# Performance work log

Measured on AMD Instinct MI355X. Metric: run time of the kernel, lower is better.

Reference implementation:

```python
import jax, jax.numpy as jnp
import numpy as np

B, IN, OUT, T = 64, 1024, 512, 512
V_TH = 1.0
TAU = 16.0


def alpha_kernel(t, tau):
    # SRM alpha kernel: (t/tau)*exp(1 - t/tau) for t > 0, else 0.
    # Mask BEFORE exp to avoid overflow for large negative t.
    ts = jnp.where(t > 0, t, tau)
    v = (ts / tau) * jnp.exp(1.0 - ts / tau)
    return jnp.where(t > 0, v, 0.0)


def setup_inputs() -> dict:
    key = jax.random.key(0)
    k1, k2 = jax.random.split(key)
    # input spike times in [0, T/2)
    in_spike = jax.random.uniform(k1, (B, IN), dtype=jnp.float32) * (T / 2)
    weight = jax.random.normal(k2, (OUT, IN), dtype=jnp.float32) / np.float32(np.sqrt(IN))
    return {"in_spike": in_spike, "weight": weight}


def reference(in_spike, weight):
    t_seq = jnp.arange(T, dtype=jnp.float32)                  # [T]
    time_sequence = t_seq[None, None, :] - in_spike[:, :, None]  # [B, in, T]
    v_input = alpha_kernel(time_sequence, TAU)                 # [B, in, T]
    # fc applied along the `in` axis at every time step
    membrane_voltage = jnp.einsum('bit,oi->bot', v_input, weight)  # [B, out, T]
    # first time index where voltage crosses threshold; T if never.
    mask = membrane_voltage >= V_TH                            # [B, out, T]
    spiked = mask.any(axis=-1)
    first_t = jnp.argmax(mask, axis=-1)                        # first True index
    out_spike = jnp.where(spiked, first_t, T).astype(jnp.float32)  # [B, out]
    return out_spike
```

## Files before the change

kernel.cpp:

```cpp
#include <hip/hip_runtime.h>
#include <math.h>

#define BATCH   64
#define INS     1024
#define OUTS    512
#define TSTEPS  512
#define TAUF    16.0f
#define LOG2E_OVER_TAU 0.0901684400555602f

#define TT 64
#define NTRANS ((INS / TT) * (OUTS / TT))

__global__ __launch_bounds__(256) void pre_kernel(
        const float* __restrict__ w, float* __restrict__ wT,
        const float* __restrict__ in_spike, float4* __restrict__ spk,
        int* __restrict__ starts) {
    __shared__ float tile[TT][TT + 1];
    __shared__ int hist[257];
    __shared__ int cursor[257];
    __shared__ int wsum[4];

    if (blockIdx.x < NTRANS) {
        const int i0 = (blockIdx.x & (INS / TT - 1)) * TT;
        const int o0 = (blockIdx.x / (INS / TT)) * TT;
        const int c  = threadIdx.x & 63;
        const int r  = threadIdx.x >> 6;
#pragma unroll
        for (int rr = r; rr < TT; rr += 4)
            tile[rr][c] = w[(o0 + rr) * INS + i0 + c];
        __syncthreads();
#pragma unroll
        for (int rr = r; rr < TT; rr += 4)
            wT[(i0 + rr) * OUTS + o0 + c] = tile[c][rr];
        return;
    }

    const int b = blockIdx.x - NTRANS;
    const int tid = threadIdx.x;
    for (int k = tid; k < 257; k += 256) hist[k] = 0;
    __syncthreads();

    float sv[INS / 256];
    int   tv[INS / 256];
#pragma unroll
    for (int j = 0; j < INS / 256; ++j) {
        int i = tid + j * 256;
        float s = in_spike[b * INS + i];
        sv[j] = s;
        int t = (int)floorf(s) + 1;
        t = t < 1 ? 1 : (t > 256 ? 256 : t);
        tv[j] = t;
        atomicAdd(&hist[t], 1);
    }
    __syncthreads();

    const int lane = tid & 63;
    const int wv   = tid >> 6;
    int v = hist[tid + 1];
    int sc = v;
#pragma unroll
    for (int off = 1; off < 64; off <<= 1) {
        int n = __shfl_up(sc, off, 64);
        if (lane >= off) sc += n;
    }
    if (lane == 63) wsum[wv] = sc;
    __syncthreads();
    int base = 0;
    for (int j = 0; j < wv; ++j) base += wsum[j];
    int excl = sc + base - v;
    cursor[tid + 1] = excl;
    starts[b * 258 + tid + 1] = excl;
    if (tid == 0) { starts[b * 258] = 0; starts[b * 258 + 257] = INS; }
    __syncthreads();

#pragma unroll
    for (int j = 0; j < INS / 256; ++j) {
        int i = tid + j * 256;
        int t = tv[j];
        int pos = atomicAdd(&cursor[t], 1);
        float A = expf(fmaf(sv[j], 1.0f / TAUF, 1.0f)) * (1.0f / TAUF);
        float C = -sv[j] * A;
        spk[b * INS + pos] =
            make_float4(A, __int_as_float(i * (OUTS / 2)), C, __int_as_float(t));
    }
}

#define OL 32
#define G  32
#define WS 8
#define TAIL0 257

__global__ __launch_bounds__(OL * G, 8) void spike_scan_kernel(
        const float4* __restrict__ spk, const int* __restrict__ starts,
        const float* __restrict__ wT, float* __restrict__ out) {
    const int b = blockIdx.x;
    const int x = threadIdx.x;
    const int g = threadIdx.y;
    const int tid = g * OL + x;

    __shared__ float4 sspk[INS];
    __shared__ float2 psP0[G][OL];
    __shared__ float2 psP1[G][OL];
    __shared__ int    sSt[258];
    __shared__ int    sFirst[2 * OL];

    sspk[tid] = spk[b * INS + tid];
    if (tid < 258) sSt[tid] = starts[b * 258 + tid];
    if (tid < 2 * OL) sFirst[tid] = TSTEPS;
    __syncthreads();

    const int w0 = g * WS + 1;
    const int kBeg = sSt[w0];
    const int kEnd = sSt[w0 + WS];
    const float2* __restrict__ wT2x = (const float2*)wT + (blockIdx.y * OL + x);

    float pA0 = 0.f, pC0 = 0.f, pA1 = 0.f, pC1 = 0.f;
    float rA0 = 0.f, rC0 = 0.f, rA1 = 0.f, rC1 = 0.f;
    int k = kBeg;
    for (; k + 8 <= kEnd; k += 8) {
        float4 p0 = sspk[k + 0];
        float4 p1 = sspk[k + 1];
        float4 p2 = sspk[k + 2];
        float4 p3 = sspk[k + 3];
        float4 p4 = sspk[k + 4];
        float4 p5 = sspk[k + 5];
        float4 p6 = sspk[k + 6];
        float4 p7 = sspk[k + 7];
        float2 q0 = wT2x[__float_as_int(p0.y)];
        float2 q1 = wT2x[__float_as_int(p1.y)];
        float2 q2 = wT2x[__float_as_int(p2.y)];
        float2 q3 = wT2x[__float_as_int(p3.y)];
        float2 q4 = wT2x[__float_as_int(p4.y)];
        float2 q5 = wT2x[__float_as_int(p5.y)];
        float2 q6 = wT2x[__float_as_int(p6.y)];
        float2 q7 = wT2x[__float_as_int(p7.y)];
        pA0 = fmaf(q0.x, p0.x, pA0); pC0 = fmaf(q0.x, p0.z, pC0);
        pA1 = fmaf(q0.y, p0.x, pA1); pC1 = fmaf(q0.y, p0.z, pC1);
        pA0 = fmaf(q1.x, p1.x, pA0); pC0 = fmaf(q1.x, p1.z, pC0);
        pA1 = fmaf(q1.y, p1.x, pA1); pC1 = fmaf(q1.y, p1.z, pC1);
        pA0 = fmaf(q2.x, p2.x, pA0); pC0 = fmaf(q2.x, p2.z, pC0);
        pA1 = fmaf(q2.y, p2.x, pA1); pC1 = fmaf(q2.y, p2.z, pC1);
        pA0 = fmaf(q3.x, p3.x, pA0); pC0 = fmaf(q3.x, p3.z, pC0);
        pA1 = fmaf(q3.y, p3.x, pA1); pC1 = fmaf(q3.y, p3.z, pC1);
        rA0 = fmaf(q4.x, p4.x, rA0); rC0 = fmaf(q4.x, p4.z, rC0);
        rA1 = fmaf(q4.y, p4.x, rA1); rC1 = fmaf(q4.y, p4.z, rC1);
        rA0 = fmaf(q5.x, p5.x, rA0); rC0 = fmaf(q5.x, p5.z, rC0);
        rA1 = fmaf(q5.y, p5.x, rA1); rC1 = fmaf(q5.y, p5.z, rC1);
        rA0 = fmaf(q6.x, p6.x, rA0); rC0 = fmaf(q6.x, p6.z, rC0);
        rA1 = fmaf(q6.y, p6.x, rA1); rC1 = fmaf(q6.y, p6.z, rC1);
        rA0 = fmaf(q7.x, p7.x, rA0); rC0 = fmaf(q7.x, p7.z, rC0);
        rA1 = fmaf(q7.y, p7.x, rA1); rC1 = fmaf(q7.y, p7.z, rC1);
    }
    for (; k < kEnd; ++k) {
        float4 p = sspk[k];
        float2 q = wT2x[__float_as_int(p.y)];
        pA0 = fmaf(q.x, p.x, pA0); pC0 = fmaf(q.x, p.z, pC0);
        pA1 = fmaf(q.y, p.x, pA1); pC1 = fmaf(q.y, p.z, pC1);
    }
    pA0 += rA0; pC0 += rC0; pA1 += rA1; pC1 += rC1;
    psP0[g][x] = make_float2(pA0, pC0);
    psP1[g][x] = make_float2(pA1, pC1);
    __syncthreads();

    float SA0 = 0.f, SC0 = 0.f, SA1 = 0.f, SC1 = 0.f;
    for (int j = 0; j < g; ++j) {
        float2 a = psP0[j][x];
        float2 c = psP1[j][x];
        SA0 += a.x; SC0 += a.y; SA1 += c.x; SC1 += c.y;
    }
    float TA0 = SA0, TC0 = SC0, TA1 = SA1, TC1 = SC1;
    for (int j = g; j < G; ++j) {
        float2 a = psP0[j][x];
        float2 c = psP1[j][x];
        TA0 += a.x; TC0 += a.y; TA1 += c.x; TC1 += c.y;
    }

    unsigned m0 = 0, m1 = 0;
    float tf = (float)w0;
    k = kBeg;
    for (int d = 0; d < WS; ++d) {
        int e = sSt[w0 + d + 1];
        float dA0 = 0.f, dC0 = 0.f, dA1 = 0.f, dC1 = 0.f;
        while (k < e) {
            float4 p = sspk[k];
            float2 q = wT2x[__float_as_int(p.y)];
            dA0 = fmaf(q.x, p.x, dA0); dC0 = fmaf(q.x, p.z, dC0);
            dA1 = fmaf(q.y, p.x, dA1); dC1 = fmaf(q.y, p.z, dC1);
            ++k;
        }
        SA0 += dA0; SC0 += dC0; SA1 += dA1; SC1 += dC1;
        float ev = exp2f(tf * LOG2E_OVER_TAU);
        m0 |= (fmaf(tf, SA0, SC0) >= ev) ? (1u << d) : 0u;
        m1 |= (fmaf(tf, SA1, SC1) >= ev) ? (1u << d) : 0u;
        tf += 1.0f;
    }
    int f0 = m0 ? (w0 + __builtin_ffs(m0) - 1) : TSTEPS;
    int f1 = m1 ? (w0 + __builtin_ffs(m1) - 1) : TSTEPS;

    {
        const int t0 = TAIL0 + g * WS;
        unsigned n0 = 0, n1 = 0;
        float tg = (float)t0;
        for (int d = 0; d < WS; ++d) {
            if (t0 + d < TSTEPS) {
                float ev = exp2f(tg * LOG2E_OVER_TAU);
                n0 |= (fmaf(tg, TA0, TC0) >= ev) ? (1u << d) : 0u;
                n1 |= (fmaf(tg, TA1, TC1) >= ev) ? (1u << d) : 0u;
            }
            tg += 1.0f;
        }
        if (n0) f0 = min(f0, t0 + __builtin_ffs(n0) - 1);
        if (n1) f1 = min(f1, t0 + __builtin_ffs(n1) - 1);
    }

    if (f0 < TSTEPS) atomicMin(&sFirst[2 * x], f0);
    if (f1 < TSTEPS) atomicMin(&sFirst[2 * x + 1], f1);
    __syncthreads();
    if (tid < 2 * OL)
        out[b * OUTS + blockIdx.y * (2 * OL) + tid] = (float)sFirst[tid];
}

extern "C" void kernel_launch(void* const* d_in, const int* in_sizes, int n_in,
                              void* d_out, int out_size, void* d_ws, size_t ws_size,
                              hipStream_t stream) {
    const float* in_spike = (const float*)d_in[0];
    const float* weight   = (const float*)d_in[1];
    float* out = (float*)d_out;

    float*  wT     = (float*)d_ws;
    float4* spk    = (float4*)((char*)d_ws + (size_t)INS * OUTS * sizeof(float));
    int*    starts = (int*)((char*)d_ws + (size_t)INS * OUTS * sizeof(float)
                                        + (size_t)BATCH * INS * sizeof(float4));

    pre_kernel<<<NTRANS + BATCH, 256, 0, stream>>>(weight, wT, in_spike, spk, starts);
    spike_scan_kernel<<<dim3(BATCH, OUTS / (2 * OL)), dim3(OL, G), 0, stream>>>(
        spk, starts, wT, out);
}
```

Before: 92.36 us.

## Single pass over spike buckets, saving per-step local voltages for threshold check

```diff
diff --git a/kernel.cpp b/kernel.cpp
--- a/kernel.cpp
+++ b/kernel.cpp
@@ -110,56 +110,50 @@
     __syncthreads();
 
     const int w0 = g * WS + 1;
-    const int kBeg = sSt[w0];
-    const int kEnd = sSt[w0 + WS];
     const float2* __restrict__ wT2x = (const float2*)wT + (blockIdx.y * OL + x);
 
-    float pA0 = 0.f, pC0 = 0.f, pA1 = 0.f, pC1 = 0.f;
-    float rA0 = 0.f, rC0 = 0.f, rA1 = 0.f, rC1 = 0.f;
-    int k = kBeg;
-    for (; k + 8 <= kEnd; k += 8) {
-        float4 p0 = sspk[k + 0];
-        float4 p1 = sspk[k + 1];
-        float4 p2 = sspk[k + 2];
-        float4 p3 = sspk[k + 3];
-        float4 p4 = sspk[k + 4];
-        float4 p5 = sspk[k + 5];
-        float4 p6 = sspk[k + 6];
-        float4 p7 = sspk[k + 7];
-        float2 q0 = wT2x[__float_as_int(p0.y)];
-        float2 q1 = wT2x[__float_as_int(p1.y)];
-        float2 q2 = wT2x[__float_as_int(p2.y)];
-        float2 q3 = wT2x[__float_as_int(p3.y)];
-        float2 q4 = wT2x[__float_as_int(p4.y)];
-        float2 q5 = wT2x[__float_as_int(p5.y)];
-        float2 q6 = wT2x[__float_as_int(p6.y)];
-        float2 q7 = wT2x[__float_as_int(p7.y)];
-        pA0 = fmaf(q0.x, p0.x, pA0); pC0 = fmaf(q0.x, p0.z, pC0);
-        pA1 = fmaf(q0.y, p0.x, pA1); pC1 = fmaf(q0.y, p0.z, pC1);
-        pA0 = fmaf(q1.x, p1.x, pA0); pC0 = fmaf(q1.x, p1.z, pC0);
-        pA1 = fmaf(q1.y, p1.x, pA1); pC1 = fmaf(q1.y, p1.z, pC1);
-        pA0 = fmaf(q2.x, p2.x, pA0); pC0 = fmaf(q2.x, p2.z, pC0);
-        pA1 = fmaf(q2.y, p2.x, pA1); pC1 = fmaf(q2.y, p2.z, pC1);
-        pA0 = fmaf(q3.x, p3.x, pA0); pC0 = fmaf(q3.x, p3.z, pC0);
-        pA1 = fmaf(q3.y, p3.x, pA1); pC1 = fmaf(q3.y, p3.z, pC1);
-        rA0 = fmaf(q4.x, p4.x, rA0); rC0 = fmaf(q4.x, p4.z, rC0);
-        rA1 = fmaf(q4.y, p4.x, rA1); rC1 = fmaf(q4.y, p4.z, rC1);
-        rA0 = fmaf(q5.x, p5.x, rA0); rC0 = fmaf(q5.x, p5.z, rC0);
-        rA1 = fmaf(q5.y, p5.x, rA1); rC1 = fmaf(q5.y, p5.z, rC1);
-        rA0 = fmaf(q6.x, p6.x, rA0); rC0 = fmaf(q6.x, p6.z, rC0);
-        rA1 = fmaf(q6.y, p6.x, rA1); rC1 = fmaf(q6.y, p6.z, rC1);
-        rA0 = fmaf(q7.x, p7.x, rA0); rC0 = fmaf(q7.x, p7.z, rC0);
-        rA1 = fmaf(q7.y, p7.x, rA1); rC1 = fmaf(q7.y, p7.z, rC1);
-    }
-    for (; k < kEnd; ++k) {
-        float4 p = sspk[k];
-        float2 q = wT2x[__float_as_int(p.y)];
-        pA0 = fmaf(q.x, p.x, pA0); pC0 = fmaf(q.x, p.z, pC0);
-        pA1 = fmaf(q.y, p.x, pA1); pC1 = fmaf(q.y, p.z, pC1);
-    }
-    pA0 += rA0; pC0 += rC0; pA1 += rA1; pC1 += rC1;
-    psP0[g][x] = make_float2(pA0, pC0);
-    psP1[g][x] = make_float2(pA1, pC1);
+    float cA0 = 0.f, cC0 = 0.f, cA1 = 0.f, cC1 = 0.f;
+    float l00, l01, l02, l03, l04, l05, l06, l07;
+    float l10, l11, l12, l13, l14, l15, l16, l17;
+    int k = sSt[w0];
+
+#define BUCKET(D, LA, LB)                                                     \
+    {                                                                         \
+        const int e = sSt[w0 + (D) + 1];                                      \
+        for (; k + 2 <= e; k += 2) {                                          \
+            float4 p0 = sspk[k + 0];                                          \
+            float4 p1 = sspk[k + 1];                                          \
+            float2 q0 = wT2x[__float_as_int(p0.y)];                           \
+            float2 q1 = wT2x[__float_as_int(p1.y)];                           \
+            cA0 = fmaf(q0.x, p0.x, cA0); cC0 = fmaf(q0.x, p0.z, cC0);         \
+            cA1 = fmaf(q0.y, p0.x, cA1); cC1 = fmaf(q0.y, p0.z, cC1);         \
+            cA0 = fmaf(q1.x, p1.x, cA0); cC0 = fmaf(q1.x, p1.z, cC0);         \
+            cA1 = fmaf(q1.y, p1.x, cA1); cC1 = fmaf(q1.y, p1.z, cC1);         \
+        }                                                                     \
+        if (k < e) {                                                          \
+            float4 p = sspk[k];                                               \
+            float2 q = wT2x[__float_as_int(p.y)];                             \
+            cA0 = fmaf(q.x, p.x, cA0); cC0 = fmaf(q.x, p.z, cC0);             \
+            cA1 = fmaf(q.y, p.x, cA1); cC1 = fmaf(q.y, p.z, cC1);             \
+            ++k;                                                              \
+        }                                                                     \
+        const float tf = (float)(w0 + (D));                                   \
+        LA = fmaf(tf, cA0, cC0);                                              \
+        LB = fmaf(tf, cA1, cC1);                                              \
+    }
+
+    BUCKET(0, l00, l10)
+    BUCKET(1, l01, l11)
+    BUCKET(2, l02, l12)
+    BUCKET(3, l03, l13)
+    BUCKET(4, l04, l14)
+    BUCKET(5, l05, l15)
+    BUCKET(6, l06, l16)
+    BUCKET(7, l07, l17)
+#undef BUCKET
+
+    psP0[g][x] = make_float2(cA0, cC0);
+    psP1[g][x] = make_float2(cA1, cC1);
     __syncthreads();
 
     float SA0 = 0.f, SC0 = 0.f, SA1 = 0.f, SC1 = 0.f;
@@ -176,24 +170,22 @@
     }
 
     unsigned m0 = 0, m1 = 0;
-    float tf = (float)w0;
-    k = kBeg;
-    for (int d = 0; d < WS; ++d) {
-        int e = sSt[w0 + d + 1];
-        float dA0 = 0.f, dC0 = 0.f, dA1 = 0.f, dC1 = 0.f;
-        while (k < e) {
-            float4 p = sspk[k];
-            float2 q = wT2x[__float_as_int(p.y)];
-            dA0 = fmaf(q.x, p.x, dA0); dC0 = fmaf(q.x, p.z, dC0);
-            dA1 = fmaf(q.y, p.x, dA1); dC1 = fmaf(q.y, p.z, dC1);
-            ++k;
-        }
-        SA0 += dA0; SC0 += dC0; SA1 += dA1; SC1 += dC1;
-        float ev = exp2f(tf * LOG2E_OVER_TAU);
-        m0 |= (fmaf(tf, SA0, SC0) >= ev) ? (1u << d) : 0u;
-        m1 |= (fmaf(tf, SA1, SC1) >= ev) ? (1u << d) : 0u;
-        tf += 1.0f;
-    }
+#define CHECK(D, LA, LB)                                                      \
+    {                                                                         \
+        const float tf = (float)(w0 + (D));                                   \
+        const float ev = exp2f(tf * LOG2E_OVER_TAU);                          \
+        m0 |= (fmaf(tf, SA0, SC0) + (LA) >= ev) ? (1u << (D)) : 0u;           \
+        m1 |= (fmaf(tf, SA1, SC1) + (LB) >= ev) ? (1u << (D)) : 0u;           \
+    }
+    CHECK(0, l00, l10)
+    CHECK(1, l01, l11)
+    CHECK(2, l02, l12)
+    CHECK(3, l03, l13)
+    CHECK(4, l04, l14)
+    CHECK(5, l05, l15)
+    CHECK(6, l06, l16)
+    CHECK(7, l07, l17)
+#undef CHECK
     int f0 = m0 ? (w0 + __builtin_ffs(m0) - 1) : TSTEPS;
     int f1 = m1 ? (w0 + __builtin_ffs(m1) - 1) : TSTEPS;
 
```

Result: faster. 81.51 us, median of 2 (-11.8%).
